# Optimization experiments

Hardware: AMD Instinct MI355X
Metric: run time of the kernel (lower is better)

Reference implementation:

```python
import jax, jax.numpy as jnp
import numpy as np

EPS = 1e-6

def _ln(x, g, b):
    m = jnp.mean(x, -1, keepdims=True)
    v = jnp.mean((x - m) ** 2, -1, keepdims=True)
    return (x - m) * jax.lax.rsqrt(v + 1e-5) * g + b

def _mha(qin, kin, vin, wq, bq, wk, bk, wv, bv, wo, bo, nh=8):
    B, T, D = qin.shape
    S = kin.shape[1]
    dh = D // nh
    q = (qin @ wq + bq).reshape(B, T, nh, dh)
    k = (kin @ wk + bk).reshape(B, S, nh, dh)
    v = (vin @ wv + bv).reshape(B, S, nh, dh)
    a = jax.nn.softmax(jnp.einsum('bthd,bshd->bhts', q, k) / np.float32(np.sqrt(dh)), -1)
    o = jnp.einsum('bhts,bshd->bthd', a, v).reshape(B, T, D)
    return o @ wo + bo

def _sinu_pe(pos, num_feats=128, temperature=20.0):
    # pos: [..., 2] (x, y); returns [..., 2*num_feats] ordered (y-feats, x-feats)
    dim_t = temperature ** ((2 * (jnp.arange(num_feats) // 2)) / num_feats)
    e = pos[..., None] * (2 * np.pi) / dim_t  # [..., 2, F]
    e = jnp.stack([jnp.sin(e[..., 0::2]), jnp.cos(e[..., 1::2])], -1).reshape(e.shape)
    return jnp.concatenate([e[..., 1, :], e[..., 0, :]], -1)

def _spatial36(b1, b2, sizes):
    # b1, b2: [B, Q, 4]; sizes: [B, 2] = (h, w). UPT-style 18 feats + log -> 36.
    h = sizes[:, 0:1]; w = sizes[:, 1:2]
    c1x = (b1[..., 0] + b1[..., 2]) / 2; c1y = (b1[..., 1] + b1[..., 3]) / 2
    c2x = (b2[..., 0] + b2[..., 2]) / 2; c2y = (b2[..., 1] + b2[..., 3]) / 2
    w1 = b1[..., 2] - b1[..., 0]; h1 = b1[..., 3] - b1[..., 1]
    w2 = b2[..., 2] - b2[..., 0]; h2 = b2[..., 3] - b2[..., 1]
    a1 = w1 * h1; a2 = w2 * h2
    dx = jnp.abs(c2x - c1x) / (w1 + EPS)
    dy = jnp.abs(c2y - c1y) / (h1 + EPS)
    ix = jnp.clip(jnp.minimum(b1[..., 2], b2[..., 2]) - jnp.maximum(b1[..., 0], b2[..., 0]), 0)
    iy = jnp.clip(jnp.minimum(b1[..., 3], b2[..., 3]) - jnp.maximum(b1[..., 1], b2[..., 1]), 0)
    inter = ix * iy
    iou = inter / (a1 + a2 - inter + EPS)
    f = jnp.stack([c1x / w, c1y / h, c2x / w, c2y / h, w1 / w, h1 / h, w2 / w, h2 / h,
                   a1 / (h * w), a2 / (h * w), a2 / (a1 + EPS), w1 / (h1 + EPS), w2 / (h2 + EPS), iou,
                   (c2x > c1x) * dx, (c2x < c1x) * dx, (c2y > c1y) * dy, (c2y < c1y) * dy], -1)
    return jnp.concatenate([f, jnp.log(f + EPS)], -1)

def _forward(boxes, embeds, image_sizes, pose, line, sw1, sb1, sw2, sb2, sw3, sb3, bw, bb, pw, pb, lw, lb, enc_pe_w, enc_pe_b, enc_qkv_w, enc_qkv_b, enc_out_w, enc_out_b, enc_ff1_w, enc_ff1_b, enc_ff2_w, enc_ff2_b, enc_ln1_g, enc_ln1_b, enc_ln2_g, enc_ln2_b, dec_q_w, dec_q_b, dec_kv_w, dec_kv_b, dec_out_w, dec_out_b, dec_ff1_w, dec_ff1_b, dec_ff2_w, dec_ff2_b, dec_ln1_g, dec_ln1_b, dec_ln2_g, dec_ln2_b, fc1_w, fc1_b, fc2_w, fc2_b, mln1_g, mln1_b, mln2_g, mln2_b, m1_w, m1_b, m2_w, m2_b, labels, nh):
    B, N, _ = boxes.shape
    # static human-object pairing (x != y) & (x < nh)
    xg, yg = np.meshgrid(np.arange(N), np.arange(N), indexing='ij')
    keep = (xg != yg) & (xg < nh)
    xk = jnp.asarray(xg[keep]); yk = jnp.asarray(yg[keep])  # [P]
    # line features: adaptive-avg-pool(1,1) + 1x1 conv == spatial mean + linear
    line_feat = jnp.mean(line, axis=(2, 3)) @ lw + lb  # [B, 256]
    # spatial head on all N*N ordered pairs, then gather kept pairs
    xa = jnp.asarray(xg.reshape(-1)); ya = jnp.asarray(yg.reshape(-1))
    f36 = _spatial36(boxes[:, xa], boxes[:, ya], image_sizes)  # [B, N*N, 36]
    s = jax.nn.relu(f36 @ sw1 + sb1)
    s = jax.nn.relu(s @ sw2 + sb2)
    s = jax.nn.relu(s @ sw3 + sb3)
    spa = s.reshape(B, N, N, -1)[:, xk, yk]  # [B, P, R]
    # box sinusoidal positional encodings (cat of centre-PE and wh-PE)
    whwh = image_sizes[:, jnp.array([1, 0, 1, 0])][:, None]  # [B,1,4]
    bxn = boxes / whwh
    ctr = (bxn[..., :2] + bxn[..., 2:]) / 2
    whb = bxn[..., 2:] - bxn[..., :2]
    box_pe = jnp.concatenate([_sinu_pe(ctr), _sinu_pe(whb)], -1)  # [B, N, 512]
    # 2-layer transformer encoder over instance tokens (pos added to q,k)
    posx = box_pe @ enc_pe_w + enc_pe_b
    x = embeds
    for i in range(enc_qkv_w.shape[0]):
        wq, wk_, wv = jnp.split(enc_qkv_w[i], 3, axis=1)
        bq, bk_, bv = jnp.split(enc_qkv_b[i], 3)
        qk = x + posx
        att = _mha(qk, qk, x, wq, bq, wk_, bk_, wv, bv, enc_out_w[i], enc_out_b[i])
        x = _ln(x + att, enc_ln1_g[i], enc_ln1_b[i])
        ff = jax.nn.relu(x @ enc_ff1_w[i] + enc_ff1_b[i]) @ enc_ff2_w[i] + enc_ff2_b[i]
        x = _ln(x + ff, enc_ln2_g[i], enc_ln2_b[i])
    # pair gather + human/object positional embeds (box PE projected + line feature)
    pe_h = box_pe[:, xk] @ bw + bb + line_feat[:, None, :]
    pe_o = box_pe[:, yk] @ bw + bb + line_feat[:, None, :]
    h = x[:, xk]; o = x[:, yk]  # [B, P, 256]
    pose_ctx = pose @ pw + pb  # [B, M, 256]
    # HO refine decoder: cross-attention from pair tokens to pose tokens
    for l in range(dec_q_w.shape[0]):
        wk_, wv = jnp.split(dec_kv_w[l], 2, axis=1)
        bk_, bv = jnp.split(dec_kv_b[l], 2)
        def _layer(feat, pe):
            att = _mha(feat + pe, pose_ctx, pose_ctx, dec_q_w[l], dec_q_b[l], wk_, bk_, wv, bv, dec_out_w[l], dec_out_b[l])
            feat = _ln(feat + att, dec_ln1_g[l], dec_ln1_b[l])
            ff = jax.nn.relu(feat @ dec_ff1_w[l] + dec_ff1_b[l]) @ dec_ff2_w[l] + dec_ff2_b[l]
            return _ln(feat + ff, dec_ln2_g[l], dec_ln2_b[l])
        h = _layer(h, pe_h)
        o = _layer(o, pe_o)
    # multi-modal fusion
    ho = jnp.concatenate([h, o], -1)  # [B, P, 512]
    ho = _ln(ho @ fc1_w + fc1_b, mln1_g, mln1_b)
    sp = _ln(spa @ fc2_w + fc2_b, mln2_g, mln2_b)
    z = jax.nn.relu(jnp.concatenate([ho, sp], -1))
    z = jax.nn.relu(z @ m1_w + m1_b)
    z = jax.nn.relu(z @ m2_w + m2_b)
    return z  # [B, P, 256] HOI query features

def setup_inputs() -> dict:
    key = jax.random.key(0)
    ks = iter(jax.random.split(key, 80))
    B, N, NH, M, HH, WW = 16, 128, 32, 64, 8, 8
    W = 0.05
    def rn(shape, s=1.0):
        return jax.random.normal(next(ks), shape, dtype=jnp.float32) * s
    def ru(shape):
        return jax.random.uniform(next(ks), shape, dtype=jnp.float32)
    sizes = 800.0 + 480.0 * ru((B, 2))  # (h, w)
    wh = sizes[:, jnp.array([1, 0])]
    xy = ru((B, N, 2)) * wh[:, None] * 0.7
    bwh = ru((B, N, 2)) * wh[:, None] * 0.25 + 4.0
    boxes = jnp.concatenate([xy, xy + bwh], -1)
    labels = jnp.concatenate([jnp.zeros((B, NH), jnp.int32), jax.random.randint(next(ks), (B, N - NH), 1, 81, dtype=jnp.int32)], -1)
    return dict(
        boxes=boxes, embeds=rn((B, N, 256)), image_sizes=sizes, pose=rn((B, M, 768)), line=rn((B, 2048, HH, WW)),
        sw1=rn((36, 128), W), sb1=jnp.zeros((128,)), sw2=rn((128, 256), W), sb2=jnp.zeros((256,)), sw3=rn((256, 256), W), sb3=jnp.zeros((256,)),
        bw=rn((512, 256), W), bb=jnp.zeros((256,)), pw=rn((768, 256), W), pb=jnp.zeros((256,)), lw=rn((2048, 256), W), lb=jnp.zeros((256,)),
        enc_pe_w=rn((512, 256), W), enc_pe_b=jnp.zeros((256,)),
        enc_qkv_w=rn((2, 256, 768), W), enc_qkv_b=jnp.zeros((2, 768)), enc_out_w=rn((2, 256, 256), W), enc_out_b=jnp.zeros((2, 256)),
        enc_ff1_w=rn((2, 256, 1024), W), enc_ff1_b=jnp.zeros((2, 1024)), enc_ff2_w=rn((2, 1024, 256), W), enc_ff2_b=jnp.zeros((2, 256)),
        enc_ln1_g=jnp.ones((2, 256)), enc_ln1_b=jnp.zeros((2, 256)), enc_ln2_g=jnp.ones((2, 256)), enc_ln2_b=jnp.zeros((2, 256)),
        dec_q_w=rn((2, 256, 256), W), dec_q_b=jnp.zeros((2, 256)), dec_kv_w=rn((2, 256, 512), W), dec_kv_b=jnp.zeros((2, 512)),
        dec_out_w=rn((2, 256, 256), W), dec_out_b=jnp.zeros((2, 256)),
        dec_ff1_w=rn((2, 256, 1024), W), dec_ff1_b=jnp.zeros((2, 1024)), dec_ff2_w=rn((2, 1024, 256), W), dec_ff2_b=jnp.zeros((2, 256)),
        dec_ln1_g=jnp.ones((2, 256)), dec_ln1_b=jnp.zeros((2, 256)), dec_ln2_g=jnp.ones((2, 256)), dec_ln2_b=jnp.zeros((2, 256)),
        fc1_w=rn((512, 256), W), fc1_b=jnp.zeros((256,)), fc2_w=rn((256, 256), W), fc2_b=jnp.zeros((256,)),
        mln1_g=jnp.ones((256,)), mln1_b=jnp.zeros((256,)), mln2_g=jnp.ones((256,)), mln2_b=jnp.zeros((256,)),
        m1_w=rn((512, 384), W), m1_b=jnp.zeros((384,)), m2_w=rn((384, 256), W), m2_b=jnp.zeros((256,)),
        labels=labels, nh=NH)

def reference(boxes, embeds, image_sizes, pose, line, sw1, sb1, sw2, sb2, sw3, sb3, bw, bb, pw, pb, lw, lb, enc_pe_w, enc_pe_b, enc_qkv_w, enc_qkv_b, enc_out_w, enc_out_b, enc_ff1_w, enc_ff1_b, enc_ff2_w, enc_ff2_b, enc_ln1_g, enc_ln1_b, enc_ln2_g, enc_ln2_b, dec_q_w, dec_q_b, dec_kv_w, dec_kv_b, dec_out_w, dec_out_b, dec_ff1_w, dec_ff1_b, dec_ff2_w, dec_ff2_b, dec_ln1_g, dec_ln1_b, dec_ln2_g, dec_ln2_b, fc1_w, fc1_b, fc2_w, fc2_b, mln1_g, mln1_b, mln2_g, mln2_b, m1_w, m1_b, m2_w, m2_b, labels, nh):
    return _forward(boxes, embeds, image_sizes, pose, line, sw1, sb1, sw2, sb2, sw3, sb3, bw, bb, pw, pb, lw, lb, enc_pe_w, enc_pe_b, enc_qkv_w, enc_qkv_b, enc_out_w, enc_out_b, enc_ff1_w, enc_ff1_b, enc_ff2_w, enc_ff2_b, enc_ln1_g, enc_ln1_b, enc_ln2_g, enc_ln2_b, dec_q_w, dec_q_b, dec_kv_w, dec_kv_b, dec_out_w, dec_out_b, dec_ff1_w, dec_ff1_b, dec_ff2_w, dec_ff2_b, dec_ln1_g, dec_ln1_b, dec_ln2_g, dec_ln2_b, fc1_w, fc1_b, fc2_w, fc2_b, mln1_g, mln1_b, mln2_g, mln2_b, m1_w, m1_b, m2_w, m2_b, labels, nh)
```

## Files before the change

### kernel.cpp

```cpp
#include <hip/hip_runtime.h>
#include <stdint.h>

static constexpr int B      = 16;
static constexpr int N      = 128;
static constexpr int P      = 4064;
static constexpr int MPOSE  = 64;
static constexpr int64_t BN = (int64_t)B * N;
static constexpr int64_t BP = (int64_t)B * P;

#define TWO_PI 6.283185307179586f
#define QSCALE 0.17677669529663687f

typedef __attribute__((ext_vector_type(4))) float f32x4;
typedef __attribute__((ext_vector_type(8))) short bf16x8;
typedef __attribute__((ext_vector_type(8))) unsigned short u16x8;
typedef __attribute__((ext_vector_type(4))) unsigned short u16x4;

__device__ __forceinline__ unsigned short f2bf(float f) {
    union { float f; unsigned u; } v; v.f = f;
    unsigned r = (v.u + 0x7fffu + ((v.u >> 16) & 1u)) >> 16;
    return (unsigned short)r;
}
__device__ __forceinline__ float bf2f(unsigned short u) {
    union { unsigned u; float f; } v; v.u = (unsigned)u << 16;
    return v.f;
}
__device__ __forceinline__ void pair_xy(int p, int& x, int& y) {
    x = p / 127;
    int r = p - x * 127;
    y = (r < x) ? r : r + 1;
}
__device__ __forceinline__ int xcd_swz(int orig, int nwg) {
    int q = nwg >> 3, r = nwg & 7;
    int xcd = orig & 7, idx = orig >> 3;
    return (xcd < r ? xcd * (q + 1) : r * (q + 1) + (xcd - r) * q) + idx;
}
__device__ __forceinline__ void gld16(const unsigned short* g, unsigned short* l) {
    __builtin_amdgcn_global_load_lds(
        (const __attribute__((address_space(1))) void*)g,
        (__attribute__((address_space(3))) void*)l, 16, 0, 0);
}

struct WDesc { const float* src; int64_t dstOff; int K, Nn, Kpad, blockStart; };
struct WTable { WDesc d[29]; int nDesc; };

__global__ __launch_bounds__(256) void wprep_all_k(WTable t, unsigned short* __restrict__ wt)
{
    __shared__ float s[32][33];
    int bid = blockIdx.x;
    int di = 0;
    for (int i = 1; i < t.nDesc; ++i) if (t.d[i].blockStart <= bid) di = i;
    const WDesc& d = t.d[di];
    int lbid = bid - d.blockStart;
    int kTiles = d.Kpad >> 5;
    int k0 = (lbid % kTiles) * 32, n0 = (lbid / kTiles) * 32;
    int tx = threadIdx.x & 31, ty = threadIdx.x >> 5;
#pragma unroll
    for (int i = 0; i < 4; ++i) {
        int k = k0 + ty + i * 8;
        s[ty + i * 8][tx] = (k < d.K) ? d.src[(int64_t)k * d.Nn + n0 + tx] : 0.f;
    }
    __syncthreads();
    unsigned short* dst = wt + d.dstOff;
#pragma unroll
    for (int i = 0; i < 4; ++i) {
        int n = n0 + ty + i * 8;
        dst[(int64_t)n * d.Kpad + k0 + tx] = f2bf(s[tx][ty + i * 8]);
    }
}

template <bool RELU_OUT>
__global__ __launch_bounds__(256) void bgemm_k(
    const float* __restrict__ A, const float* __restrict__ A2, int lda,
    const unsigned short* __restrict__ Bt, int ldk,
    const float* __restrict__ bias,
    const float* __restrict__ Cadd, int addStride, int addCols,
    const float* __restrict__ lfp,
    float* __restrict__ C, int ldc,
    int kSteps)
{
    __shared__ unsigned short As[128][40];
    __shared__ unsigned short Bs[128][40];
    const int tid  = threadIdx.x;
    const int lane = tid & 63;
    const int wave = tid >> 6;
    const int wr = wave >> 1, wc = wave & 1;
    const int row0 = blockIdx.y * 128, col0 = blockIdx.x * 128;
    const int l15 = lane & 15, l4 = lane >> 4;
    const int sr = tid >> 1;
    const int sh = (tid & 1) * 16;

    f32x4 acc[4][4] = {};

    for (int ks = 0; ks < kSteps; ++ks) {
        const int k0 = ks * 32;
        {
            const int64_t off = (int64_t)(row0 + sr) * lda + k0 + sh;
            const float* ap = A + off;
            float v[16];
#pragma unroll
            for (int i = 0; i < 4; ++i) {
                float4 tv = ((const float4*)ap)[i];
                v[i*4+0] = tv.x; v[i*4+1] = tv.y; v[i*4+2] = tv.z; v[i*4+3] = tv.w;
            }
            if (A2) {
                const float* ap2 = A2 + off;
#pragma unroll
                for (int i = 0; i < 4; ++i) {
                    float4 tv = ((const float4*)ap2)[i];
                    v[i*4+0] += tv.x; v[i*4+1] += tv.y; v[i*4+2] += tv.z; v[i*4+3] += tv.w;
                }
            }
            u16x8 p0, p1;
#pragma unroll
            for (int j = 0; j < 8; ++j) { p0[j] = f2bf(v[j]); p1[j] = f2bf(v[8 + j]); }
            *(u16x8*)&As[sr][sh]     = p0;
            *(u16x8*)&As[sr][sh + 8] = p1;
        }
        {
            const unsigned short* bp = Bt + (int64_t)(col0 + sr) * ldk + k0 + sh;
            *(u16x8*)&Bs[sr][sh]     = *(const u16x8*)bp;
            *(u16x8*)&Bs[sr][sh + 8] = *(const u16x8*)(bp + 8);
        }
        __syncthreads();
        bf16x8 af[4], bfr[4];
#pragma unroll
        for (int f = 0; f < 4; ++f) {
            af[f]  = *(const bf16x8*)&As[wr * 64 + f * 16 + l15][l4 * 8];
            bfr[f] = *(const bf16x8*)&Bs[wc * 64 + f * 16 + l15][l4 * 8];
        }
#pragma unroll
        for (int i = 0; i < 4; ++i)
#pragma unroll
            for (int j = 0; j < 4; ++j)
                acc[i][j] = __builtin_amdgcn_mfma_f32_16x16x32_bf16(af[i], bfr[j], acc[i][j], 0, 0, 0);
        __syncthreads();
    }
#pragma unroll
    for (int i = 0; i < 4; ++i) {
        int rb = row0 + wr * 64 + i * 16 + l4 * 4;
#pragma unroll
        for (int j = 0; j < 4; ++j) {
            int c = col0 + wc * 64 + j * 16 + l15;
            float bv = bias ? bias[c] : 0.f;
#pragma unroll
            for (int e = 0; e < 4; ++e) {
                int r = rb + e;
                float vv = acc[i][j][e] + bv;
                if (Cadd && c < addCols) vv += Cadd[(int64_t)r * addStride + c];
                if (lfp) vv += lfp[(r >> 7) * 256 + c];
                if (RELU_OUT) vv = fmaxf(vv, 0.f);
                C[(int64_t)r * ldc + c] = vv;
            }
        }
    }
}

static void bgemm(hipStream_t st,
                  const float* A, const float* A2, int lda,
                  const unsigned short* Bt, int ldk, const float* bias,
                  const float* Cadd, int addStride, int addCols, const float* lfp,
                  float* C, int ldc, int M, int Ncols, int K, bool reluOut)
{
    dim3 g(Ncols / 128, M / 128), b(256);
    if (reluOut) bgemm_k<true><<<g,b,0,st>>>(A,A2,lda,Bt,ldk,bias,Cadd,addStride,addCols,lfp,C,ldc,K/32);
    else         bgemm_k<false><<<g,b,0,st>>>(A,A2,lda,Bt,ldk,bias,Cadd,addStride,addCols,lfp,C,ldc,K/32);
}

__global__ __launch_bounds__(256) void tgemm16_k(
    const float* __restrict__ A, int lda,
    const unsigned short* __restrict__ Bt, int ldk,
    const float* __restrict__ bias,
    const float* __restrict__ res,
    const float* __restrict__ g, const float* __restrict__ be,
    float* __restrict__ C, int kSteps)
{
    __shared__ unsigned short As[16][40];
    __shared__ unsigned short Bs[256][40];
    __shared__ float partS[16][4], partQ[16][4];
    __shared__ float statM[16], statI[16];
    const int tid = threadIdx.x;
    const int lane = tid & 63, w = tid >> 6;
    const int l15 = lane & 15, l4 = lane >> 4;
    const int row0 = blockIdx.x * 16;

    f32x4 acc[4] = {};
    for (int ks = 0; ks < kSteps; ++ks) {
        int k0 = ks * 32;
        if (tid < 64) {
            const float* ap = A + (int64_t)(row0 + (tid >> 2)) * lda + k0 + (tid & 3) * 8;
            float4 t0 = ((const float4*)ap)[0];
            float4 t1 = ((const float4*)ap)[1];
            u16x8 p;
            p[0]=f2bf(t0.x); p[1]=f2bf(t0.y); p[2]=f2bf(t0.z); p[3]=f2bf(t0.w);
            p[4]=f2bf(t1.x); p[5]=f2bf(t1.y); p[6]=f2bf(t1.z); p[7]=f2bf(t1.w);
            *(u16x8*)&As[tid >> 2][(tid & 3) * 8] = p;
        }
        {
            const unsigned short* bp = Bt + (int64_t)tid * ldk + k0;
#pragma unroll
            for (int q = 0; q < 4; ++q)
                *(u16x8*)&Bs[tid][q * 8] = *(const u16x8*)(bp + q * 8);
        }
        __syncthreads();
        bf16x8 af = *(const bf16x8*)&As[l15][l4 * 8];
        bf16x8 bfr[4];
#pragma unroll
        for (int f = 0; f < 4; ++f)
            bfr[f] = *(const bf16x8*)&Bs[w * 64 + f * 16 + l15][l4 * 8];
#pragma unroll
        for (int j = 0; j < 4; ++j)
            acc[j] = __builtin_amdgcn_mfma_f32_16x16x32_bf16(af, bfr[j], acc[j], 0, 0, 0);
        __syncthreads();
    }
    float ps[4] = {}, pq[4] = {};
#pragma unroll
    for (int j = 0; j < 4; ++j) {
        int c = w * 64 + j * 16 + l15;
#pragma unroll
        for (int e = 0; e < 4; ++e) {
            int r = l4 * 4 + e;
            float v = acc[j][e] + bias[c] + res[(int64_t)(row0 + r) * 256 + c];
            acc[j][e] = v;
            ps[e] += v;
            pq[e] += v * v;
        }
    }
#pragma unroll
    for (int e = 0; e < 4; ++e) {
#pragma unroll
        for (int m = 1; m < 16; m <<= 1) {
            ps[e] += __shfl_xor(ps[e], m);
            pq[e] += __shfl_xor(pq[e], m);
        }
    }
    if (l15 == 0) {
#pragma unroll
        for (int e = 0; e < 4; ++e) {
            int r = l4 * 4 + e;
            partS[r][w] = ps[e];
            partQ[r][w] = pq[e];
        }
    }
    __syncthreads();
    if (tid < 16) {
        float s = partS[tid][0] + partS[tid][1] + partS[tid][2] + partS[tid][3];
        float q = partQ[tid][0] + partQ[tid][1] + partQ[tid][2] + partQ[tid][3];
        float m = s * (1.f/256.f);
        float var = q * (1.f/256.f) - m * m;
        statM[tid] = m;
        statI[tid] = rsqrtf(var + 1e-5f);
    }
    __syncthreads();
#pragma unroll
    for (int j = 0; j < 4; ++j) {
        int c = w * 64 + j * 16 + l15;
#pragma unroll
        for (int e = 0; e < 4; ++e) {
            int r = l4 * 4 + e;
            C[(int64_t)(row0 + r) * 256 + c] = (acc[j][e] - statM[r]) * statI[r] * g[c] + be[c];
        }
    }
}

template <bool RELU_OUT, bool OUT_BF16>
__global__ __launch_bounds__(256) void hgemm_k(
    const unsigned short* __restrict__ A, int lda,
    const unsigned short* __restrict__ Bt, int ldk,
    const float* __restrict__ bias,
    void* __restrict__ Cv, int ldc,
    int kSteps, int nx)
{
    __shared__ unsigned short As[2][128][32];
    __shared__ unsigned short Bs[2][128][32];
    const int tid  = threadIdx.x;
    const int lane = tid & 63;
    const int wave = tid >> 6;
    const int wr = wave >> 1, wc = wave & 1;
    const int wgid = xcd_swz(blockIdx.x, gridDim.x);
    const int row0 = (wgid / nx) * 128, col0 = (wgid % nx) * 128;
    const int l15 = lane & 15, l4 = lane >> 4;
    const int srow = lane >> 2;
    const int scol = (lane & 3) * 8;

    f32x4 acc[4][4] = {};

    {
        const int k0 = 0;
#pragma unroll
        for (int i = 0; i < 2; ++i) {
            int seg = wave * 2 + i;
            int r = seg * 16 + srow;
            gld16(A  + (int64_t)(row0 + r) * lda + k0 + scol, &As[0][seg * 16][0]);
            gld16(Bt + (int64_t)(col0 + r) * ldk + k0 + scol, &Bs[0][seg * 16][0]);
        }
    }
    asm volatile("s_waitcnt vmcnt(0)" ::: "memory");
    __builtin_amdgcn_s_barrier();
    asm volatile("" ::: "memory");

    int cur = 0;
    for (int ks = 0; ks < kSteps; ++ks) {
        if (ks + 1 < kSteps) {
            const int k0n = (ks + 1) * 32;
            const int nb = cur ^ 1;
#pragma unroll
            for (int i = 0; i < 2; ++i) {
                int seg = wave * 2 + i;
                int r = seg * 16 + srow;
                gld16(A  + (int64_t)(row0 + r) * lda + k0n + scol, &As[nb][seg * 16][0]);
                gld16(Bt + (int64_t)(col0 + r) * ldk + k0n + scol, &Bs[nb][seg * 16][0]);
            }
        }
        bf16x8 af[4], bfr[4];
#pragma unroll
        for (int f = 0; f < 4; ++f) {
            af[f]  = *(const bf16x8*)&As[cur][wr * 64 + f * 16 + l15][l4 * 8];
            bfr[f] = *(const bf16x8*)&Bs[cur][wc * 64 + f * 16 + l15][l4 * 8];
        }
#pragma unroll
        for (int i = 0; i < 4; ++i)
#pragma unroll
            for (int j = 0; j < 4; ++j)
                acc[i][j] = __builtin_amdgcn_mfma_f32_16x16x32_bf16(af[i], bfr[j], acc[i][j], 0, 0, 0);
        asm volatile("s_waitcnt vmcnt(0)" ::: "memory");
        __builtin_amdgcn_s_barrier();
        asm volatile("" ::: "memory");
        cur ^= 1;
    }
#pragma unroll
    for (int i = 0; i < 4; ++i) {
        int rb = row0 + wr * 64 + i * 16 + l4 * 4;
#pragma unroll
        for (int j = 0; j < 4; ++j) {
            int c = col0 + wc * 64 + j * 16 + l15;
            float bv = bias ? bias[c] : 0.f;
#pragma unroll
            for (int e = 0; e < 4; ++e) {
                int64_t off = (int64_t)(rb + e) * ldc + c;
                float vv = acc[i][j][e] + bv;
                if (RELU_OUT) vv = fmaxf(vv, 0.f);
                if (OUT_BF16) ((unsigned short*)Cv)[off] = f2bf(vv);
                else          ((float*)Cv)[off] = vv;
            }
        }
    }
}

__global__ __launch_bounds__(256) void spa_k(
    const float* __restrict__ boxes, const float* __restrict__ sizes,
    const unsigned short* __restrict__ W1, const float* __restrict__ b1,
    const unsigned short* __restrict__ W2, const float* __restrict__ b2,
    unsigned short* __restrict__ t3out, int chunk0)
{
    __shared__ unsigned short F[128][72];
    __shared__ unsigned short Bs[128][40];
    __shared__ unsigned short D1s[128][136];
    const int tid  = threadIdx.x;
    const int lane = tid & 63;
    const int wave = tid >> 6;
    const int wr = wave >> 1, wc = wave & 1;
    const int row0 = blockIdx.x * 128;
    const int l15 = lane & 15, l4 = lane >> 4;
    const int sr = tid >> 1;
    const int sh = (tid & 1) * 16;

    if (tid < 128) {
        int gp = chunk0 + row0 + tid;
        int b = gp / P, p = gp - b * P;
        int xi, yi; pair_xy(p, xi, yi);
        const float* b1x = boxes + ((int64_t)b * N + xi) * 4;
        const float* b2x = boxes + ((int64_t)b * N + yi) * 4;
        float h = sizes[b * 2 + 0], w = sizes[b * 2 + 1];
        float c1x = (b1x[0] + b1x[2]) * 0.5f, c1y = (b1x[1] + b1x[3]) * 0.5f;
        float c2x = (b2x[0] + b2x[2]) * 0.5f, c2y = (b2x[1] + b2x[3]) * 0.5f;
        float w1 = b1x[2] - b1x[0], h1 = b1x[3] - b1x[1];
        float w2 = b2x[2] - b2x[0], h2 = b2x[3] - b2x[1];
        float a1 = w1 * h1, a2 = w2 * h2;
        float dx = fabsf(c2x - c1x) / (w1 + 1e-6f);
        float dy = fabsf(c2y - c1y) / (h1 + 1e-6f);
        float ix = fmaxf(fminf(b1x[2], b2x[2]) - fmaxf(b1x[0], b2x[0]), 0.f);
        float iy = fmaxf(fminf(b1x[3], b2x[3]) - fmaxf(b1x[1], b2x[1]), 0.f);
        float inter = ix * iy;
        float iou = inter / (a1 + a2 - inter + 1e-6f);
        float f[18];
        f[0] = c1x / w;  f[1] = c1y / h;  f[2] = c2x / w;  f[3] = c2y / h;
        f[4] = w1 / w;   f[5] = h1 / h;   f[6] = w2 / w;   f[7] = h2 / h;
        f[8] = a1 / (h * w); f[9] = a2 / (h * w); f[10] = a2 / (a1 + 1e-6f);
        f[11] = w1 / (h1 + 1e-6f); f[12] = w2 / (h2 + 1e-6f); f[13] = iou;
        f[14] = (c2x > c1x) ? dx : 0.f;  f[15] = (c2x < c1x) ? dx : 0.f;
        f[16] = (c2y > c1y) ? dy : 0.f;  f[17] = (c2y < c1y) ? dy : 0.f;
#pragma unroll
        for (int i = 0; i < 18; ++i) {
            F[tid][i]      = f2bf(f[i]);
            F[tid][18 + i] = f2bf(logf(f[i] + 1e-6f));
        }
#pragma unroll
        for (int i = 36; i < 64; ++i) F[tid][i] = 0;
    }
    __syncthreads();

    f32x4 acc1[4][4] = {};
    for (int ks = 0; ks < 2; ++ks) {
        const int k0 = ks * 32;
        {
            const unsigned short* bp = W1 + (int64_t)sr * 64 + k0 + sh;
            *(u16x8*)&Bs[sr][sh]     = *(const u16x8*)bp;
            *(u16x8*)&Bs[sr][sh + 8] = *(const u16x8*)(bp + 8);
        }
        __syncthreads();
        bf16x8 af[4], bfr[4];
#pragma unroll
        for (int f = 0; f < 4; ++f) {
            af[f]  = *(const bf16x8*)&F[wr * 64 + f * 16 + l15][k0 + l4 * 8];
            bfr[f] = *(const bf16x8*)&Bs[wc * 64 + f * 16 + l15][l4 * 8];
        }
#pragma unroll
        for (int i = 0; i < 4; ++i)
#pragma unroll
            for (int j = 0; j < 4; ++j)
                acc1[i][j] = __builtin_amdgcn_mfma_f32_16x16x32_bf16(af[i], bfr[j], acc1[i][j], 0, 0, 0);
        __syncthreads();
    }
#pragma unroll
    for (int i = 0; i < 4; ++i) {
        int rb = wr * 64 + i * 16 + l4 * 4;
#pragma unroll
        for (int j = 0; j < 4; ++j) {
            int c = wc * 64 + j * 16 + l15;
            float bv = b1[c];
#pragma unroll
            for (int e = 0; e < 4; ++e)
                D1s[rb + e][c] = f2bf(fmaxf(acc1[i][j][e] + bv, 0.f));
        }
    }
    __syncthreads();

    f32x4 acc2[2][4][4] = {};
#pragma unroll
    for (int n = 0; n < 2; ++n) {
        for (int kk = 0; kk < 4; ++kk) {
            {
                const unsigned short* bp = W2 + (int64_t)(n * 128 + sr) * 128 + kk * 32 + sh;
                *(u16x8*)&Bs[sr][sh]     = *(const u16x8*)bp;
                *(u16x8*)&Bs[sr][sh + 8] = *(const u16x8*)(bp + 8);
            }
            __syncthreads();
            bf16x8 af[4], bfr[4];
#pragma unroll
            for (int f = 0; f < 4; ++f) {
                af[f]  = *(const bf16x8*)&D1s[wr * 64 + f * 16 + l15][kk * 32 + l4 * 8];
                bfr[f] = *(const bf16x8*)&Bs[wc * 64 + f * 16 + l15][l4 * 8];
            }
#pragma unroll
            for (int i = 0; i < 4; ++i)
#pragma unroll
                for (int j = 0; j < 4; ++j)
                    acc2[n][i][j] = __builtin_amdgcn_mfma_f32_16x16x32_bf16(af[i], bfr[j], acc2[n][i][j], 0, 0, 0);
            __syncthreads();
        }
    }
#pragma unroll
    for (int n = 0; n < 2; ++n)
#pragma unroll
    for (int i = 0; i < 4; ++i) {
        int rb = row0 + wr * 64 + i * 16 + l4 * 4;
#pragma unroll
        for (int j = 0; j < 4; ++j) {
            int c = n * 128 + wc * 64 + j * 16 + l15;
            float bv = b2[c];
#pragma unroll
            for (int e = 0; e < 4; ++e)
                t3out[(int64_t)(rb + e) * 256 + c] = f2bf(fmaxf(acc2[n][i][j][e] + bv, 0.f));
        }
    }
}

__global__ __launch_bounds__(256) void zprep_k(
    const float* __restrict__ UV, const float* __restrict__ fb,
    const unsigned short* __restrict__ t3,
    const float* __restrict__ g1, const float* __restrict__ be1,
    const float* __restrict__ g2, const float* __restrict__ be2,
    unsigned short* __restrict__ zb, int chunk0, int rows)
{
    int wave = threadIdx.x >> 6, lane = threadIdx.x & 63;
    int li = blockIdx.x * 4 + wave;
    if (li >= rows) return;
    int gp = chunk0 + li;
    int b = gp / P, p = gp - b * P;
    int xi, yi; pair_xy(p, xi, yi);
    int c = lane * 4;
    {
        float4 u  = *(const float4*)(UV + ((int64_t)(b * 128 + xi)) * 512 + c);
        float4 vv = *(const float4*)(UV + ((int64_t)(b * 128 + yi)) * 512 + 256 + c);
        float4 fbv = *(const float4*)(fb + c);
        float4 v;
        v.x = u.x + vv.x + fbv.x; v.y = u.y + vv.y + fbv.y;
        v.z = u.z + vv.z + fbv.z; v.w = u.w + vv.w + fbv.w;
        float s  = v.x + v.y + v.z + v.w;
        float sq = v.x*v.x + v.y*v.y + v.z*v.z + v.w*v.w;
#pragma unroll
        for (int off = 1; off < 64; off <<= 1) {
            s  += __shfl_xor(s, off);
            sq += __shfl_xor(sq, off);
        }
        float m = s * (1.f/256.f);
        float var = sq * (1.f/256.f) - m * m;
        float inv = rsqrtf(var + 1e-5f);
        float4 gg = *(const float4*)(g1 + c);
        float4 bb = *(const float4*)(be1 + c);
        u16x4 o;
        o[0] = f2bf(fmaxf((v.x - m) * inv * gg.x + bb.x, 0.f));
        o[1] = f2bf(fmaxf((v.y - m) * inv * gg.y + bb.y, 0.f));
        o[2] = f2bf(fmaxf((v.z - m) * inv * gg.z + bb.z, 0.f));
        o[3] = f2bf(fmaxf((v.w - m) * inv * gg.w + bb.w, 0.f));
        *(u16x4*)(zb + (int64_t)li * 512 + c) = o;
    }
    {
        u16x4 u = *(const u16x4*)(t3 + (int64_t)li * 256 + c);
        float4 v;
        v.x = bf2f(u[0]); v.y = bf2f(u[1]); v.z = bf2f(u[2]); v.w = bf2f(u[3]);
        float s  = v.x + v.y + v.z + v.w;
        float sq = v.x*v.x + v.y*v.y + v.z*v.z + v.w*v.w;
#pragma unroll
        for (int off = 1; off < 64; off <<= 1) {
            s  += __shfl_xor(s, off);
            sq += __shfl_xor(sq, off);
        }
        float m = s * (1.f/256.f);
        float var = sq * (1.f/256.f) - m * m;
        float inv = rsqrtf(var + 1e-5f);
        float4 gg = *(const float4*)(g2 + c);
        float4 bb = *(const float4*)(be2 + c);
        u16x4 o;
        o[0] = f2bf(fmaxf((v.x - m) * inv * gg.x + bb.x, 0.f));
        o[1] = f2bf(fmaxf((v.y - m) * inv * gg.y + bb.y, 0.f));
        o[2] = f2bf(fmaxf((v.z - m) * inv * gg.z + bb.z, 0.f));
        o[3] = f2bf(fmaxf((v.w - m) * inv * gg.w + bb.w, 0.f));
        *(u16x4*)(zb + (int64_t)li * 512 + 256 + c) = o;
    }
}

__global__ __launch_bounds__(256) void line_mean_k(const float* __restrict__ line, float* __restrict__ lm)
{
    int wave = threadIdx.x >> 6, lane = threadIdx.x & 63;
    int bc = blockIdx.x * 4 + wave;
    float v = line[(int64_t)bc * 64 + lane];
#pragma unroll
    for (int off = 1; off < 64; off <<= 1) v += __shfl_xor(v, off);
    if (lane == 0) lm[bc] = v * (1.f/64.f);
}

__global__ __launch_bounds__(256) void line_proj_k(
    const float* __restrict__ lm, const float* __restrict__ lw,
    const float* __restrict__ lb, float* __restrict__ lf)
{
    __shared__ float red[8][32];
    int b = blockIdx.y, jg = blockIdx.x;
    int jj = threadIdx.x & 31, cc = threadIdx.x >> 5;
    int j = jg * 32 + jj;
    const float* lmb = lm + (int64_t)b * 2048 + cc * 256;
    const float* lwp = lw + (int64_t)(cc * 256) * 256 + j;
    float acc = 0.f;
#pragma unroll 4
    for (int k = 0; k < 256; ++k) acc += lmb[k] * lwp[(int64_t)k * 256];
    red[cc][jj] = acc;
    __syncthreads();
    if (cc == 0) {
        float s = lb[j];
#pragma unroll
        for (int i = 0; i < 8; ++i) s += red[i][jj];
        lf[b * 256 + j] = s;
    }
}

__global__ __launch_bounds__(512) void boxpe_k(
    const float* __restrict__ boxes, const float* __restrict__ sizes, float* __restrict__ boxpe)
{
    int row = blockIdx.x;
    int b = row >> 7;
    int i = threadIdx.x;
    const float* bx = boxes + (int64_t)row * 4;
    float h = sizes[b * 2 + 0], w = sizes[b * 2 + 1];
    float x0 = bx[0] / w, y0 = bx[1] / h, x1 = bx[2] / w, y1 = bx[3] / h;
    int seg = i >> 7, j = i & 127, k = j >> 1;
    float val;
    switch (seg) {
        case 0: val = (y0 + y1) * 0.5f; break;
        case 1: val = (x0 + x1) * 0.5f; break;
        case 2: val = (y1 - y0); break;
        default: val = (x1 - x0); break;
    }
    float dimt = exp2f((float)k * (4.321928094887362f / 64.f));
    float arg = val * TWO_PI / dimt;
    boxpe[(int64_t)row * 512 + i] = (j & 1) ? cosf(arg) : sinf(arg);
}

__global__ __launch_bounds__(128) void enc_attn_k(
    const float* __restrict__ qkv, float* __restrict__ outp)
{
    int b = blockIdx.x >> 3, hd = blockIdx.x & 7;
    __shared__ float kl[128][32];
    __shared__ float vl[128][32];
    int tid = threadIdx.x;
    for (int i = tid; i < 128 * 32; i += 128) {
        int s = i >> 5, j = i & 31;
        const float* rp = qkv + ((int64_t)(b * 128 + s)) * 768 + hd * 32 + j;
        kl[s][j] = rp[256];
        vl[s][j] = rp[512];
    }
    __syncthreads();
    int t = tid;
    const float* qp = qkv + ((int64_t)(b * 128 + t)) * 768 + hd * 32;
    float qr[32];
#pragma unroll
    for (int j = 0; j < 32; ++j) qr[j] = qp[j] * QSCALE;
    float m = -1e30f, l = 0.f;
    for (int s = 0; s < 128; ++s) {
        float d = 0.f;
#pragma unroll
        for (int j = 0; j < 32; ++j) d += qr[j] * kl[s][j];
        float mn = fmaxf(m, d);
        l = l * __expf(m - mn) + __expf(d - mn);
        m = mn;
    }
    float acc[32] = {};
    for (int s = 0; s < 128; ++s) {
        float d = 0.f;
#pragma unroll
        for (int j = 0; j < 32; ++j) d += qr[j] * kl[s][j];
        float wgt = __expf(d - m);
#pragma unroll
        for (int j = 0; j < 32; ++j) acc[j] += wgt * vl[s][j];
    }
    float linv = 1.f / l;
    float* op = outp + ((int64_t)(b * 128 + t)) * 256 + hd * 32;
#pragma unroll
    for (int j = 0; j < 32; ++j) op[j] = acc[j] * linv;
}

__global__ __launch_bounds__(256) void dec_attn_k(
    const float* __restrict__ q, const float* __restrict__ kv, int ldkv,
    float* __restrict__ outp, int rows, int rpb)
{
    int hd = blockIdx.y;
    int r0 = blockIdx.x * 256;
    __shared__ float kl[2][64][32];
    __shared__ float vl[2][64][32];
    int tid = threadIdx.x;
    int b0 = r0 / rpb;
    int b1 = (r0 + 255) / rpb;
    if (b1 >= B) b1 = B - 1;
    for (int i = tid; i < 64 * 32; i += 256) {
        int s = i >> 5, j = i & 31;
        int64_t off0 = ((int64_t)(b0 * MPOSE + s)) * ldkv + hd * 32 + j;
        int64_t off1 = ((int64_t)(b1 * MPOSE + s)) * ldkv + hd * 32 + j;
        kl[0][s][j] = kv[off0];
        vl[0][s][j] = kv[off0 + 256];
        kl[1][s][j] = kv[off1];
        vl[1][s][j] = kv[off1 + 256];
    }
    __syncthreads();
    int r = r0 + tid;
    if (r >= rows) return;
    int which = (r / rpb == b0) ? 0 : 1;
    int64_t qoff = (int64_t)r * 256 + hd * 32;
    float qr[32];
#pragma unroll
    for (int j = 0; j < 32; ++j) qr[j] = q[qoff + j] * QSCALE;
    float m = -1e30f, l = 0.f;
    for (int s = 0; s < 64; ++s) {
        float d = 0.f;
#pragma unroll
        for (int j = 0; j < 32; ++j) d += qr[j] * kl[which][s][j];
        float mn = fmaxf(m, d);
        l = l * __expf(m - mn) + __expf(d - mn);
        m = mn;
    }
    float acc[32] = {};
    for (int s = 0; s < 64; ++s) {
        float d = 0.f;
#pragma unroll
        for (int j = 0; j < 32; ++j) d += qr[j] * kl[which][s][j];
        float wgt = __expf(d - m);
#pragma unroll
        for (int j = 0; j < 32; ++j) acc[j] += wgt * vl[which][s][j];
    }
    float linv = 1.f / l;
#pragma unroll
    for (int j = 0; j < 32; ++j) outp[qoff + j] = acc[j] * linv;
}

static constexpr int64_t WT_QKV  = 0;
static constexpr int64_t WT_EOUT = WT_QKV  + 2*196608;
static constexpr int64_t WT_EFF1 = WT_EOUT + 2*65536;
static constexpr int64_t WT_EFF2 = WT_EFF1 + 2*262144;
static constexpr int64_t WT_DQ   = WT_EFF2 + 2*262144;
static constexpr int64_t WT_DKV  = WT_DQ   + 2*65536;
static constexpr int64_t WT_DOUT = WT_DKV  + 2*131072;
static constexpr int64_t WT_DFF1 = WT_DOUT + 2*65536;
static constexpr int64_t WT_DFF2 = WT_DFF1 + 2*262144;
static constexpr int64_t WT_SW1  = WT_DFF2 + 2*262144;
static constexpr int64_t WT_SW2  = WT_SW1 + 8192;
static constexpr int64_t WT_SW3  = WT_SW2 + 32768;
static constexpr int64_t WT_BW   = WT_SW3 + 65536;
static constexpr int64_t WT_PW   = WT_BW  + 131072;
static constexpr int64_t WT_EPE  = WT_PW  + 196608;
static constexpr int64_t WT_FC1  = WT_EPE + 131072;
static constexpr int64_t WT_FC2  = WT_FC1 + 131072;
static constexpr int64_t WT_M1   = WT_FC2 + 65536;
static constexpr int64_t WT_M2   = WT_M1  + 196608;
static constexpr int64_t WT_TOTAL = WT_M2 + 98304;

extern "C" void kernel_launch(void* const* d_in, const int* in_sizes, int n_in,
                              void* d_out, int out_size, void* d_ws, size_t ws_size,
                              hipStream_t stream)
{
    (void)in_sizes; (void)n_in; (void)out_size;
    const float* boxes     = (const float*)d_in[0];
    const float* embeds    = (const float*)d_in[1];
    const float* sizes     = (const float*)d_in[2];
    const float* pose      = (const float*)d_in[3];
    const float* line      = (const float*)d_in[4];
    const float* sw1 = (const float*)d_in[5];  const float* sb1 = (const float*)d_in[6];
    const float* sw2 = (const float*)d_in[7];  const float* sb2 = (const float*)d_in[8];
    const float* sw3 = (const float*)d_in[9];  const float* sb3 = (const float*)d_in[10];
    const float* bw  = (const float*)d_in[11]; const float* bb  = (const float*)d_in[12];
    const float* pw  = (const float*)d_in[13]; const float* pb  = (const float*)d_in[14];
    const float* lw  = (const float*)d_in[15]; const float* lb  = (const float*)d_in[16];
    const float* enc_pe_w  = (const float*)d_in[17]; const float* enc_pe_b = (const float*)d_in[18];
    const float* enc_qkv_w = (const float*)d_in[19]; const float* enc_qkv_b = (const float*)d_in[20];
    const float* enc_out_w = (const float*)d_in[21]; const float* enc_out_b = (const float*)d_in[22];
    const float* enc_ff1_w = (const float*)d_in[23]; const float* enc_ff1_b = (const float*)d_in[24];
    const float* enc_ff2_w = (const float*)d_in[25]; const float* enc_ff2_b = (const float*)d_in[26];
    const float* enc_ln1_g = (const float*)d_in[27]; const float* enc_ln1_b = (const float*)d_in[28];
    const float* enc_ln2_g = (const float*)d_in[29]; const float* enc_ln2_b = (const float*)d_in[30];
    const float* dec_q_w   = (const float*)d_in[31]; const float* dec_q_b  = (const float*)d_in[32];
    const float* dec_kv_w  = (const float*)d_in[33]; const float* dec_kv_b = (const float*)d_in[34];
    const float* dec_out_w = (const float*)d_in[35]; const float* dec_out_b = (const float*)d_in[36];
    const float* dec_ff1_w = (const float*)d_in[37]; const float* dec_ff1_b = (const float*)d_in[38];
    const float* dec_ff2_w = (const float*)d_in[39]; const float* dec_ff2_b = (const float*)d_in[40];
    const float* dec_ln1_g = (const float*)d_in[41]; const float* dec_ln1_b = (const float*)d_in[42];
    const float* dec_ln2_g = (const float*)d_in[43]; const float* dec_ln2_b = (const float*)d_in[44];
    const float* fc1_w = (const float*)d_in[45]; const float* fc1_b = (const float*)d_in[46];
    const float* fc2_w = (const float*)d_in[47]; const float* fc2_b = (const float*)d_in[48];
    const float* mln1_g = (const float*)d_in[49]; const float* mln1_b = (const float*)d_in[50];
    const float* mln2_g = (const float*)d_in[51]; const float* mln2_b = (const float*)d_in[52];
    const float* m1_w = (const float*)d_in[53]; const float* m1_b = (const float*)d_in[54];
    const float* m2_w = (const float*)d_in[55]; const float* m2_b = (const float*)d_in[56];
    float* out = (float*)d_out;

    float* base = (float*)d_ws;
    int64_t wsf = (int64_t)(ws_size / sizeof(float));
    float* x_   = base;
    float* bpw_ = x_   + 524288;
    float* lf   = bpw_ + 524288;
    float* kv0  = lf   + 4096;
    unsigned short* wt = (unsigned short*)(kv0 + 1048576);
    float* arena = (float*)(wt + WT_TOTAL);
    const int64_t LIVE_F = arena - base;
    int64_t arena_f = wsf - LIVE_F;
    if (arena_f < 0) arena_f = 0;

    float* posx  = arena;
    float* boxpe = posx  + 524288;
    float* pqkv  = boxpe + 1048576;
    float* e_qkv = pqkv  + 3145728;
    float* e_t   = e_qkv + 1572864;
    float* e_ff  = e_t   + 524288;
    float* pctx  = e_ff  + 2097152;
    float* lm    = pctx  + 262144;

    int64_t rc = ((arena_f * 2) / 1152) & ~127LL;
    if (rc > BP) rc = BP;
    if (rc < 128) rc = 128;

    {
        WTable T;
        int nd = 0, bs = 0;
        auto add = [&](const float* src, int64_t dstOff, int K, int Nn, int Kpad) {
            T.d[nd] = { src, dstOff, K, Nn, Kpad, bs };
            bs += (Kpad / 32) * (Nn / 32);
            ++nd;
        };
        for (int i = 0; i < 2; ++i) {
            add(enc_qkv_w + (int64_t)i*196608, WT_QKV  + i*196608, 256, 768, 256);
            add(enc_out_w + (int64_t)i*65536,  WT_EOUT + i*65536,  256, 256, 256);
            add(enc_ff1_w + (int64_t)i*262144, WT_EFF1 + i*262144, 256, 1024, 256);
            add(enc_ff2_w + (int64_t)i*262144, WT_EFF2 + i*262144, 1024, 256, 1024);
            add(dec_q_w   + (int64_t)i*65536,  WT_DQ   + i*65536,  256, 256, 256);
            add(dec_kv_w  + (int64_t)i*131072, WT_DKV  + i*131072, 256, 512, 256);
            add(dec_out_w + (int64_t)i*65536,  WT_DOUT + i*65536,  256, 256, 256);
            add(dec_ff1_w + (int64_t)i*262144, WT_DFF1 + i*262144, 256, 1024, 256);
            add(dec_ff2_w + (int64_t)i*262144, WT_DFF2 + i*262144, 1024, 256, 1024);
        }
        add(sw1, WT_SW1, 36, 128, 64);
        add(sw2, WT_SW2, 128, 256, 128);
        add(sw3, WT_SW3, 256, 256, 256);
        add(bw,  WT_BW,  512, 256, 512);
        add(pw,  WT_PW,  768, 256, 768);
        add(enc_pe_w, WT_EPE, 512, 256, 512);
        add(fc1_w,             WT_FC1,         256, 256, 256);
        add(fc1_w + 256 * 256, WT_FC1 + 65536, 256, 256, 256);
        add(fc2_w, WT_FC2, 256, 256, 256);
        add(m1_w, WT_M1, 512, 384, 512);
        add(m2_w, WT_M2, 384, 256, 384);
        T.nDesc = nd;
        wprep_all_k<<<bs, 256, 0, stream>>>(T, wt);
    }

    line_mean_k<<<8192, 256, 0, stream>>>(line, lm);
    line_proj_k<<<dim3(8, B), 256, 0, stream>>>(lm, lw, lb, lf);
    boxpe_k<<<(int)BN, 512, 0, stream>>>(boxes, sizes, boxpe);
    bgemm(stream, boxpe, nullptr, 512, wt + WT_EPE, 512, enc_pe_b, nullptr, 0, 0, nullptr,
          posx, 256, (int)BN, 256, 512, false);
    bgemm(stream, boxpe, nullptr, 512, wt + WT_BW,  512, bb, nullptr, 0, 0, lf,
          bpw_, 256, (int)BN, 256, 512, false);
    bgemm(stream, pose,  nullptr, 768, wt + WT_PW,  768, pb, nullptr, 0, 0, nullptr,
          pctx, 256, B*MPOSE, 256, 768, false);
    bgemm(stream, pctx, nullptr, 256, wt + WT_DKV, 256, dec_kv_b, nullptr, 0, 0, nullptr,
          kv0, 1024, B*MPOSE, 1024, 256, false);
    bgemm(stream, posx, nullptr, 256, wt + WT_QKV, 256, nullptr, nullptr, 0, 0, nullptr,
          pqkv, 1536, (int)BN, 1536, 256, false);

    for (int i = 0; i < 2; ++i) {
        const float* xin = (i == 0) ? embeds : x_;
        const unsigned short* Wq = wt + WT_QKV + (int64_t)i * 196608;
        bgemm(stream, xin, nullptr, 256, Wq, 256, enc_qkv_b + (int64_t)i*768,
              pqkv + i*768, 1536, 512, nullptr, e_qkv, 768, (int)BN, 768, 256, false);
        enc_attn_k<<<B * 8, 128, 0, stream>>>(e_qkv, e_t);
        tgemm16_k<<<(int)(BN / 16), 256, 0, stream>>>(e_t, 256, wt + WT_EOUT + (int64_t)i*65536, 256,
            enc_out_b + i*256, xin, enc_ln1_g + i*256, enc_ln1_b + i*256, x_, 8);
        bgemm(stream, x_, nullptr, 256, wt + WT_EFF1 + (int64_t)i*262144, 256, enc_ff1_b + i*1024,
              nullptr, 0, 0, nullptr, e_ff, 1024, (int)BN, 1024, 256, true);
        tgemm16_k<<<(int)(BN / 16), 256, 0, stream>>>(e_ff, 1024, wt + WT_EFF2 + (int64_t)i*262144, 1024,
            enc_ff2_b + i*256, x_, enc_ln2_g + i*256, enc_ln2_b + i*256, x_, 32);
    }

    for (int l = 0; l < 2; ++l) {
        bgemm(stream, x_, bpw_, 256, wt + WT_DQ + (int64_t)l*65536, 256, dec_q_b + l*256,
              nullptr, 0, 0, nullptr, e_t, 256, (int)BN, 256, 256, false);
        dec_attn_k<<<dim3((int)(BN / 256), 8), 256, 0, stream>>>(e_t, kv0 + l*512, 1024, e_qkv, (int)BN, N);
        tgemm16_k<<<(int)(BN / 16), 256, 0, stream>>>(e_qkv, 256, wt + WT_DOUT + (int64_t)l*65536, 256,
            dec_out_b + l*256, x_, dec_ln1_g + l*256, dec_ln1_b + l*256, x_, 8);
        bgemm(stream, x_, nullptr, 256, wt + WT_DFF1 + (int64_t)l*262144, 256, dec_ff1_b + l*1024,
              nullptr, 0, 0, nullptr, e_ff, 1024, (int)BN, 1024, 256, true);
        tgemm16_k<<<(int)(BN / 16), 256, 0, stream>>>(e_ff, 1024, wt + WT_DFF2 + (int64_t)l*262144, 1024,
            dec_ff2_b + l*256, x_, dec_ln2_g + l*256, dec_ln2_b + l*256, x_, 32);
    }
    float* UV = kv0;
    bgemm(stream, x_, nullptr, 256, wt + WT_FC1, 256, nullptr, nullptr, 0, 0, nullptr,
          UV, 512, (int)BN, 512, 256, false);

    for (int64_t c0 = 0; c0 < BP; c0 += rc) {
        int rows = (int)((BP - c0 < rc) ? (BP - c0) : rc);
        unsigned short* t3 = (unsigned short*)arena;
        unsigned short* zb = t3 + (int64_t)rc * 256;
        unsigned short* z2 = zb + (int64_t)rc * 512;

        spa_k<<<rows / 128, 256, 0, stream>>>(boxes, sizes,
            wt + WT_SW1, sb1, wt + WT_SW2, sb2, t3, (int)c0);
        hgemm_k<true,true><<<2 * (rows / 128), 256, 0, stream>>>(
            t3, 256, wt + WT_SW3, 256, sb3, z2, 256, 8, 2);
        hgemm_k<false,true><<<2 * (rows / 128), 256, 0, stream>>>(
            z2, 256, wt + WT_FC2, 256, fc2_b, t3, 256, 8, 2);
        zprep_k<<<rows / 4, 256, 0, stream>>>(UV, fc1_b, t3, mln1_g, mln1_b, mln2_g, mln2_b,
                                              zb, (int)c0, rows);
        hgemm_k<true,true><<<3 * (rows / 128), 256, 0, stream>>>(
            zb, 512, wt + WT_M1, 512, m1_b, z2, 384, 16, 3);
        hgemm_k<true,false><<<2 * (rows / 128), 256, 0, stream>>>(
            z2, 384, wt + WT_M2, 384, m2_b, out + c0 * 256, 256, 12, 2);
    }
}
```

Baseline: 795.8 us.

## Split attention head dim across 4 lanes with shuffle reductions in enc/dec attention

Each query is now handled by four threads, each owning 8 of the 32 head dimensions, and partial dot products are combined with xor shuffles. The encoder kernel launches twice as many blocks (query halves) with 256 threads, and the decoder kernel uses 64 queries per block so every block sees a single batch's K/V, which removes the dual-buffer selection. The aim is more parallelism and fewer registers per thread for these small attention kernels, at the cost of shuffle overhead and redundant K/V loads across blocks.

Result: faster. 747.7 us (-6.0%).

```diff
diff --git a/kernel.cpp b/kernel.cpp
--- a/kernel.cpp
+++ b/kernel.cpp
@@ -596,99 +596,104 @@
     boxpe[(int64_t)row * 512 + i] = (j & 1) ? cosf(arg) : sinf(arg);
 }
 
-__global__ __launch_bounds__(128) void enc_attn_k(
+__global__ __launch_bounds__(256) void enc_attn_k(
     const float* __restrict__ qkv, float* __restrict__ outp)
 {
-    int b = blockIdx.x >> 3, hd = blockIdx.x & 7;
+    int bh = blockIdx.x >> 1;
+    int qt = blockIdx.x & 1;
+    int b = bh >> 3, hd = bh & 7;
     __shared__ float kl[128][32];
     __shared__ float vl[128][32];
     int tid = threadIdx.x;
-    for (int i = tid; i < 128 * 32; i += 128) {
+    for (int i = tid; i < 128 * 32; i += 256) {
         int s = i >> 5, j = i & 31;
         const float* rp = qkv + ((int64_t)(b * 128 + s)) * 768 + hd * 32 + j;
         kl[s][j] = rp[256];
         vl[s][j] = rp[512];
     }
     __syncthreads();
-    int t = tid;
-    const float* qp = qkv + ((int64_t)(b * 128 + t)) * 768 + hd * 32;
-    float qr[32];
-#pragma unroll
-    for (int j = 0; j < 32; ++j) qr[j] = qp[j] * QSCALE;
+    int q  = qt * 64 + (tid >> 2);
+    int qu = (tid & 3) * 8;
+    const float* qp = qkv + ((int64_t)(b * 128 + q)) * 768 + hd * 32 + qu;
+    float qr[8];
+#pragma unroll
+    for (int j = 0; j < 8; ++j) qr[j] = qp[j] * QSCALE;
     float m = -1e30f, l = 0.f;
     for (int s = 0; s < 128; ++s) {
         float d = 0.f;
 #pragma unroll
-        for (int j = 0; j < 32; ++j) d += qr[j] * kl[s][j];
+        for (int j = 0; j < 8; ++j) d += qr[j] * kl[s][qu + j];
+        d += __shfl_xor(d, 1);
+        d += __shfl_xor(d, 2);
         float mn = fmaxf(m, d);
         l = l * __expf(m - mn) + __expf(d - mn);
         m = mn;
     }
-    float acc[32] = {};
+    float acc[8] = {};
     for (int s = 0; s < 128; ++s) {
         float d = 0.f;
 #pragma unroll
-        for (int j = 0; j < 32; ++j) d += qr[j] * kl[s][j];
+        for (int j = 0; j < 8; ++j) d += qr[j] * kl[s][qu + j];
+        d += __shfl_xor(d, 1);
+        d += __shfl_xor(d, 2);
         float wgt = __expf(d - m);
 #pragma unroll
-        for (int j = 0; j < 32; ++j) acc[j] += wgt * vl[s][j];
+        for (int j = 0; j < 8; ++j) acc[j] += wgt * vl[s][qu + j];
     }
     float linv = 1.f / l;
-    float* op = outp + ((int64_t)(b * 128 + t)) * 256 + hd * 32;
-#pragma unroll
-    for (int j = 0; j < 32; ++j) op[j] = acc[j] * linv;
+    float* op = outp + ((int64_t)(b * 128 + q)) * 256 + hd * 32 + qu;
+#pragma unroll
+    for (int j = 0; j < 8; ++j) op[j] = acc[j] * linv;
 }
 
 __global__ __launch_bounds__(256) void dec_attn_k(
     const float* __restrict__ q, const float* __restrict__ kv, int ldkv,
-    float* __restrict__ outp, int rows, int rpb)
+    float* __restrict__ outp, int rpb)
 {
     int hd = blockIdx.y;
-    int r0 = blockIdx.x * 256;
-    __shared__ float kl[2][64][32];
-    __shared__ float vl[2][64][32];
+    int r0 = blockIdx.x * 64;
+    int b = r0 / rpb;
+    __shared__ float kl[64][32];
+    __shared__ float vl[64][32];
     int tid = threadIdx.x;
-    int b0 = r0 / rpb;
-    int b1 = (r0 + 255) / rpb;
-    if (b1 >= B) b1 = B - 1;
     for (int i = tid; i < 64 * 32; i += 256) {
         int s = i >> 5, j = i & 31;
-        int64_t off0 = ((int64_t)(b0 * MPOSE + s)) * ldkv + hd * 32 + j;
-        int64_t off1 = ((int64_t)(b1 * MPOSE + s)) * ldkv + hd * 32 + j;
-        kl[0][s][j] = kv[off0];
-        vl[0][s][j] = kv[off0 + 256];
-        kl[1][s][j] = kv[off1];
-        vl[1][s][j] = kv[off1 + 256];
+        int64_t off = ((int64_t)(b * MPOSE + s)) * ldkv + hd * 32 + j;
+        kl[s][j] = kv[off];
+        vl[s][j] = kv[off + 256];
     }
     __syncthreads();
-    int r = r0 + tid;
-    if (r >= rows) return;
-    int which = (r / rpb == b0) ? 0 : 1;
-    int64_t qoff = (int64_t)r * 256 + hd * 32;
-    float qr[32];
-#pragma unroll
-    for (int j = 0; j < 32; ++j) qr[j] = q[qoff + j] * QSCALE;
+    int r  = r0 + (tid >> 2);
+    int qu = (tid & 3) * 8;
+    int64_t qoff = (int64_t)r * 256 + hd * 32 + qu;
+    float qr[8];
+#pragma unroll
+    for (int j = 0; j < 8; ++j) qr[j] = q[qoff + j] * QSCALE;
     float m = -1e30f, l = 0.f;
     for (int s = 0; s < 64; ++s) {
         float d = 0.f;
 #pragma unroll
-        for (int j = 0; j < 32; ++j) d += qr[j] * kl[which][s][j];
+        for (int j = 0; j < 8; ++j) d += qr[j] * kl[s][qu + j];
+        d += __shfl_xor(d, 1);
+        d += __shfl_xor(d, 2);
         float mn = fmaxf(m, d);
         l = l * __expf(m - mn) + __expf(d - mn);
         m = mn;
     }
-    float acc[32] = {};
+    float acc[8] = {};
     for (int s = 0; s < 64; ++s) {
         float d = 0.f;
 #pragma unroll
-        for (int j = 0; j < 32; ++j) d += qr[j] * kl[which][s][j];
+        for (int j = 0; j < 8; ++j) d += qr[j] * kl[s][qu + j];
+        d += __shfl_xor(d, 1);
+        d += __shfl_xor(d, 2);
         float wgt = __expf(d - m);
 #pragma unroll
-        for (int j = 0; j < 32; ++j) acc[j] += wgt * vl[which][s][j];
+        for (int j = 0; j < 8; ++j) acc[j] += wgt * vl[s][qu + j];
     }
     float linv = 1.f / l;
 #pragma unroll
-    for (int j = 0; j < 32; ++j) outp[qoff + j] = acc[j] * linv;
+    for (int j = 0; j < 8; ++j) outp[qoff + j] = acc[j] * linv;
 }
 
 static constexpr int64_t WT_QKV  = 0;
@@ -828,7 +833,7 @@
         const unsigned short* Wq = wt + WT_QKV + (int64_t)i * 196608;
         bgemm(stream, xin, nullptr, 256, Wq, 256, enc_qkv_b + (int64_t)i*768,
               pqkv + i*768, 1536, 512, nullptr, e_qkv, 768, (int)BN, 768, 256, false);
-        enc_attn_k<<<B * 8, 128, 0, stream>>>(e_qkv, e_t);
+        enc_attn_k<<<B * 8 * 2, 256, 0, stream>>>(e_qkv, e_t);
         tgemm16_k<<<(int)(BN / 16), 256, 0, stream>>>(e_t, 256, wt + WT_EOUT + (int64_t)i*65536, 256,
             enc_out_b + i*256, xin, enc_ln1_g + i*256, enc_ln1_b + i*256, x_, 8);
         bgemm(stream, x_, nullptr, 256, wt + WT_EFF1 + (int64_t)i*262144, 256, enc_ff1_b + i*1024,
@@ -840,7 +845,7 @@
     for (int l = 0; l < 2; ++l) {
         bgemm(stream, x_, bpw_, 256, wt + WT_DQ + (int64_t)l*65536, 256, dec_q_b + l*256,
               nullptr, 0, 0, nullptr, e_t, 256, (int)BN, 256, 256, false);
-        dec_attn_k<<<dim3((int)(BN / 256), 8), 256, 0, stream>>>(e_t, kv0 + l*512, 1024, e_qkv, (int)BN, N);
+        dec_attn_k<<<dim3((int)(BN / 64), 8), 256, 0, stream>>>(e_t, kv0 + l*512, 1024, e_qkv, N);
         tgemm16_k<<<(int)(BN / 16), 256, 0, stream>>>(e_qkv, 256, wt + WT_DOUT + (int64_t)l*65536, 256,
             dec_out_b + l*256, x_, dec_ln1_g + l*256, dec_ln1_b + l*256, x_, 8);
         bgemm(stream, x_, nullptr, 256, wt + WT_DFF1 + (int64_t)l*262144, 256, dec_ff1_b + l*1024,
```
